# Optimization experiments

Measured on AMD Instinct MI355X. Metric: run time of the kernel, lower is better.

## Reference

```python
import jax, jax.numpy as jnp
import numpy as np

SCALING = 32.0 / 16.0  # alpha / rank

def setup_inputs() -> dict:
    key = jax.random.key(0)
    ks = jax.random.split(key, 6)
    B, S, D_IN, D_OUT, R, N_ADAPT = 32, 1024, 1024, 4096, 16, 8
    hidden_states = jax.random.normal(ks[0], (B, S, D_IN), dtype=jnp.float32)
    adapter_ids = jax.random.randint(ks[1], (B,), 0, N_ADAPT, dtype=jnp.int32)
    W = jax.random.normal(ks[2], (D_IN, D_OUT), dtype=jnp.float32) * 0.02
    bias = jax.random.normal(ks[3], (D_OUT,), dtype=jnp.float32) * 0.02
    lora_a = jax.random.normal(ks[4], (N_ADAPT, D_IN, R), dtype=jnp.float32) * (1.0 / np.sqrt(D_IN))
    lora_b = jax.random.normal(ks[5], (N_ADAPT, R, D_OUT), dtype=jnp.float32) * 0.02
    return {"hidden_states": hidden_states, "adapter_ids": adapter_ids,
            "W": W, "bias": bias, "lora_a": lora_a, "lora_b": lora_b}

def reference(hidden_states, adapter_ids, W, bias, lora_a, lora_b):
    # Base GPT-2 Conv1D: x @ W + b, W: [in, out]
    base_out = jnp.einsum('bsd,do->bso', hidden_states, W) + bias
    # Per-sample routed LoRA: gather each sample's adapter A/B, then batched low-rank matmuls.
    # Equivalent to the torch loop over unique adapter ids with mask/scatter (dropout=0, eval).
    a_sel = lora_a[adapter_ids]  # [B, d_in, r]
    b_sel = lora_b[adapter_ids]  # [B, r, d_out]
    low_rank = jnp.einsum('bsd,bdr->bsr', hidden_states, a_sel)
    delta = jnp.einsum('bsr,bro->bso', low_rank, b_sel) * SCALING
    return base_out + delta
```

## Files before the change

### kernel.cpp

```cpp
#include <hip/hip_runtime.h>
#include <hip/hip_bf16.h>
#include <stdint.h>

constexpr int kB = 32;
constexpr int kS = 1024;
constexpr int kDin = 1024;
constexpr int kDout = 4096;
constexpr int kRank = 16;
constexpr int kNAdapt = 8;
constexpr int kM = kB * kS;
constexpr float kScale = 2.0f;

typedef __attribute__((ext_vector_type(4))) float f32x4;
typedef __attribute__((ext_vector_type(8))) short s16x8;
typedef __attribute__((ext_vector_type(8))) unsigned short u16x8;
typedef __attribute__((ext_vector_type(4))) unsigned short u16x4;

__device__ __forceinline__ unsigned short f2bf(float f) {
  union { float f; uint32_t u; } x; x.f = f;
  uint32_t u = x.u;
  u += 0x7fffu + ((u >> 16) & 1u);
  return (unsigned short)(u >> 16);
}

__global__ void cast_h_kernel(const float* __restrict__ h, unsigned short* __restrict__ out) {
  size_t i = (size_t)blockIdx.x * blockDim.x + threadIdx.x;
  const f32x4* src = reinterpret_cast<const f32x4*>(h) + i * 2;
  f32x4 v0 = src[0], v1 = src[1];
  u16x8 r;
  r[0] = f2bf(v0[0]); r[1] = f2bf(v0[1]); r[2] = f2bf(v0[2]); r[3] = f2bf(v0[3]);
  r[4] = f2bf(v1[0]); r[5] = f2bf(v1[1]); r[6] = f2bf(v1[2]); r[7] = f2bf(v1[3]);
  *reinterpret_cast<u16x8*>(out + i * 8) = r;
}

__global__ __launch_bounds__(256) void build_weff_kernel(
    const float* __restrict__ W,
    const float* __restrict__ la,
    const float* __restrict__ lb,
    unsigned short* __restrict__ weff) {
  __shared__ float Wt[64][68];
  __shared__ float At[64][20];
  __shared__ float Bt[16][68];
  int bid = blockIdx.x;
  int e = bid & 7;
  int rem = bid >> 3;
  int dt = rem >> 6;
  int ot = rem & 63;
  int d0 = dt * 64, o0 = ot * 64;
  int t = threadIdx.x;
  {
    int r = t >> 4;
    int c = (t & 15) * 4;
    const float* wp = W + (size_t)(d0 + r) * kDout + o0 + c;
#pragma unroll
    for (int p = 0; p < 4; ++p) {
      f32x4 v = *reinterpret_cast<const f32x4*>(wp + (size_t)p * 16 * kDout);
      *reinterpret_cast<f32x4*>(&Wt[p * 16 + r][c]) = v;
    }
  }
  {
    int d = t >> 2, r4 = (t & 3) * 4;
    f32x4 v = *reinterpret_cast<const f32x4*>(la + ((size_t)e * kDin + d0 + d) * kRank + r4);
    *reinterpret_cast<f32x4*>(&At[d][r4]) = v;
  }
  {
    int r = t >> 4, c = (t & 15) * 4;
    f32x4 v = *reinterpret_cast<const f32x4*>(lb + ((size_t)e * kRank + r) * kDout + o0 + c);
    *reinterpret_cast<f32x4*>(&Bt[r][c]) = v;
  }
  __syncthreads();
  int ol_base = t >> 4;
  int dl = (t & 15) * 4;
  f32x4 areg[4][4];
#pragma unroll
  for (int j = 0; j < 4; ++j)
#pragma unroll
    for (int q = 0; q < 4; ++q)
      areg[j][q] = *reinterpret_cast<const f32x4*>(&At[dl + j][q * 4]);
#pragma unroll
  for (int p = 0; p < 4; ++p) {
    int ol = p * 16 + ol_base;
    float bv[kRank];
#pragma unroll
    for (int r = 0; r < kRank; ++r) bv[r] = Bt[r][ol];
    u16x4 r4;
#pragma unroll
    for (int j = 0; j < 4; ++j) {
      float acc = 0.f;
#pragma unroll
      for (int q = 0; q < 4; ++q)
        acc += areg[j][q][0] * bv[q * 4 + 0] + areg[j][q][1] * bv[q * 4 + 1] +
               areg[j][q][2] * bv[q * 4 + 2] + areg[j][q][3] * bv[q * 4 + 3];
      r4[j] = f2bf(Wt[dl + j][ol] + kScale * acc);
    }
    *reinterpret_cast<u16x4*>(weff + ((size_t)e * kDout + o0 + ol) * kDin + d0 + dl) = r4;
  }
}

constexpr int BM = 256, BN = 256, BK = 64;
constexpr int MT2 = kM / BM;
constexpr int NT2 = kDout / BN;
constexpr int NWG2 = MT2 * NT2;
constexpr int KT = kDin / BK;

__device__ __forceinline__ void gload16(const unsigned short* g, unsigned short* l) {
  __builtin_amdgcn_global_load_lds((const __attribute__((address_space(1))) void*)g,
                                   (__attribute__((address_space(3))) void*)l, 16, 0, 0);
}

#define STG_A(slot, h, kt) do { \
  gload16(gA + (size_t)((h) * 128) * kDin + (kt) * 64, ldst + (slot) * 32768 + (h) * 8192); \
  gload16(gA + (size_t)((h) * 128 + 64) * kDin + (kt) * 64, ldst + (slot) * 32768 + (h) * 8192 + 4096); \
} while (0)
#define STG_B(slot, h, kt) do { \
  gload16(gB + (size_t)((h) * 128) * kDin + (kt) * 64, ldst + (slot) * 32768 + 16384 + (h) * 8192); \
  gload16(gB + (size_t)((h) * 128 + 64) * kDin + (kt) * 64, ldst + (slot) * 32768 + 16384 + (h) * 8192 + 4096); \
} while (0)

#define RD_A(mh) do { _Pragma("unroll") for (int i = 0; i < 4; ++i) { \
  a[i][0] = *(const s16x8*)&lds[sBase + aRow + ((mh) * 4 + i) * 1024 + e0]; \
  a[i][1] = *(const s16x8*)&lds[sBase + aRow + ((mh) * 4 + i) * 1024 + e1]; } } while (0)
#define RD_B(nh, breg) do { _Pragma("unroll") for (int j = 0; j < 2; ++j) { \
  breg[j][0] = *(const s16x8*)&lds[sBase + bRow + ((nh) * 2 + j) * 1024 + e0]; \
  breg[j][1] = *(const s16x8*)&lds[sBase + bRow + ((nh) * 2 + j) * 1024 + e1]; } } while (0)

#define MM(mh, nh, breg) do { \
  __builtin_amdgcn_s_setprio(1); \
  _Pragma("unroll") for (int i = 0; i < 4; ++i) \
  _Pragma("unroll") for (int j = 0; j < 2; ++j) { \
    acc[(mh) * 4 + i][(nh) * 2 + j] = __builtin_amdgcn_mfma_f32_16x16x32_bf16( \
        a[i][0], breg[j][0], acc[(mh) * 4 + i][(nh) * 2 + j], 0, 0, 0); \
    acc[(mh) * 4 + i][(nh) * 2 + j] = __builtin_amdgcn_mfma_f32_16x16x32_bf16( \
        a[i][1], breg[j][1], acc[(mh) * 4 + i][(nh) * 2 + j], 0, 0, 0); } \
  __builtin_amdgcn_s_setprio(0); \
} while (0)

#define BAR1() do { __builtin_amdgcn_sched_barrier(0); __builtin_amdgcn_s_barrier(); \
  asm volatile("s_waitcnt lgkmcnt(0)" ::: "memory"); __builtin_amdgcn_sched_barrier(0); } while (0)
#define BAR2() do { __builtin_amdgcn_sched_barrier(0); __builtin_amdgcn_s_barrier(); } while (0)
#define VMC(n) asm volatile("s_waitcnt vmcnt(" #n ")" ::: "memory")

#define ITER(iv, LAST_) do { \
  int kt1 = 2 * (iv) + 1, kt2 = 2 * (iv) + 2, kt3 = 2 * (iv) + 3; \
  (void)kt2; (void)kt3; \
  { int sBase = 0; RD_A(0); RD_B(0, b0); } \
  STG_B(1, 1, kt1); \
  BAR1(); MM(0, 0, b0); BAR2(); \
  { int sBase = 0; RD_B(1, b1); } \
  STG_A(1, 1, kt1); \
  BAR1(); MM(0, 1, b1); BAR2(); \
  { int sBase = 0; RD_A(1); } \
  if (!LAST_) STG_B(0, 0, kt2); \
  BAR1(); MM(1, 0, b0); BAR2(); \
  if (!LAST_) { STG_A(0, 0, kt2); VMC(4); } else { VMC(0); } \
  BAR1(); MM(1, 1, b1); BAR2(); \
  { int sBase = 32768; RD_A(0); RD_B(0, b0); } \
  if (!LAST_) STG_B(0, 1, kt2); \
  BAR1(); MM(0, 0, b0); BAR2(); \
  { int sBase = 32768; RD_B(1, b1); } \
  if (!LAST_) STG_A(0, 1, kt2); \
  BAR1(); MM(0, 1, b1); BAR2(); \
  { int sBase = 32768; RD_A(1); } \
  if (!LAST_) STG_B(1, 0, kt3); \
  BAR1(); MM(1, 0, b0); BAR2(); \
  if (!LAST_) { STG_A(1, 0, kt3); VMC(4); } \
  BAR1(); MM(1, 1, b1); BAR2(); \
} while (0)

__global__ __launch_bounds__(512, 2) void gemm256_kernel(
    const unsigned short* __restrict__ Ab,
    const unsigned short* __restrict__ Weff,
    const float* __restrict__ bias,
    const int* __restrict__ aids,
    float* __restrict__ out) {
  __shared__ unsigned short lds[65536];
  int bid = blockIdx.x;
  int swz = (bid & 7) * (NWG2 / 8) + (bid >> 3);
  int mt = swz >> 4, nt = swz & 15;
  int aid = aids[mt >> 2];
  const unsigned short* Aptr = Ab + (size_t)mt * BM * kDin;
  const unsigned short* Bptr = Weff + ((size_t)aid * kDout + (size_t)nt * BN) * kDin;

  int t = threadIdx.x;
  int l = t & 63;
  int w = t >> 6;
  int wm = w >> 2;
  int wn = w & 3;

  int srcColEl = ((t & 7) * 8) ^ (((t >> 3) & 7) << 3);
  const unsigned short* gA = Aptr + (size_t)(t >> 3) * kDin + srcColEl;
  const unsigned short* gB = Bptr + (size_t)(t >> 3) * kDin + srcColEl;
  unsigned short* ldst = lds + t * 8;

  int xmEl = (l & 7) << 3;
  int e0 = (((l >> 4) * 8) ^ xmEl);
  int e1 = e0 ^ 32;
  int aRow = (wm * 128 + (l & 15)) * 64;
  int bRow = (wn * 64 + (l & 15)) * 64 + 16384;

  f32x4 acc[8][4];
#pragma unroll
  for (int m = 0; m < 8; ++m)
#pragma unroll
    for (int n = 0; n < 4; ++n) acc[m][n] = f32x4{0.f, 0.f, 0.f, 0.f};
  s16x8 a[4][2], b0[2][2], b1[2][2];

  STG_B(0, 0, 0); STG_A(0, 0, 0); STG_B(0, 1, 0); STG_A(0, 1, 0);
  STG_B(1, 0, 1); STG_A(1, 0, 1);
  VMC(4);
  BAR2();

  for (int i = 0; i < 7; ++i) ITER(i, false);
  ITER(7, true);

  size_t row0 = (size_t)mt * BM + wm * 128 + (l >> 4) * 4;
  int col0 = nt * BN + wn * 64 + (l & 15);
#pragma unroll
  for (int nf = 0; nf < 4; ++nf) {
    float bv = bias[col0 + nf * 16];
#pragma unroll
    for (int mf = 0; mf < 8; ++mf) {
#pragma unroll
      for (int j = 0; j < 4; ++j)
        out[(row0 + mf * 16 + j) * kDout + col0 + nf * 16] = acc[mf][nf][j] + bv;
    }
  }
}

extern "C" void kernel_launch(void* const* d_in, const int* in_sizes, int n_in,
                              void* d_out, int out_size, void* d_ws, size_t ws_size,
                              hipStream_t stream) {
  const float* h    = (const float*)d_in[0];
  const int*   aids = (const int*)d_in[1];
  const float* W    = (const float*)d_in[2];
  const float* bias = (const float*)d_in[3];
  const float* la   = (const float*)d_in[4];
  const float* lb   = (const float*)d_in[5];
  float* out = (float*)d_out;

  unsigned short* Abf  = (unsigned short*)d_ws;
  unsigned short* Weff = Abf + (size_t)kM * kDin;

  cast_h_kernel<<<(kM * (size_t)kDin / 8) / 256, 256, 0, stream>>>(h, Abf);
  build_weff_kernel<<<kNAdapt * (kDin / 64) * (kDout / 64), 256, 0, stream>>>(W, la, lb, Weff);
  gemm256_kernel<<<NWG2, 512, 0, stream>>>(Abf, Weff, bias, aids, out);
}
```

Measured before the change: 460.7 us.

## Make GEMM persistent over eight N-tiles per block with cross-tile prefetch

Each workgroup now computes eight consecutive 256-wide output tiles for one M tile, which cuts the grid from 2048 to 256 blocks. The K-loop prefetch continues into the next tile's B panel and the first A k-slices, so the pipeline does not drain between tiles. The aim is to remove prologue/epilogue bubbles and launch/tail overhead, and to keep the A panel hot in cache. In exchange, the output stores are serialized inside each block, and with only 256 blocks of 512 threads some CUs may be underfilled, with poorer load balance.

```diff
diff --git a/kernel.cpp b/kernel.cpp
--- a/kernel.cpp
+++ b/kernel.cpp
@@ -100,38 +100,38 @@
 constexpr int BM = 256, BN = 256, BK = 64;
 constexpr int MT2 = kM / BM;
 constexpr int NT2 = kDout / BN;
-constexpr int NWG2 = MT2 * NT2;
-constexpr int KT = kDin / BK;
+constexpr int TPB = 8;
+constexpr int NBLK = MT2 * NT2 / TPB;
 
 __device__ __forceinline__ void gload16(const unsigned short* g, unsigned short* l) {
   __builtin_amdgcn_global_load_lds((const __attribute__((address_space(1))) void*)g,
                                    (__attribute__((address_space(3))) void*)l, 16, 0, 0);
 }
 
-#define STG_A(slot, h, kt) do { \
-  gload16(gA + (size_t)((h) * 128) * kDin + (kt) * 64, ldst + (slot) * 32768 + (h) * 8192); \
-  gload16(gA + (size_t)((h) * 128 + 64) * kDin + (kt) * 64, ldst + (slot) * 32768 + (h) * 8192 + 4096); \
+#define STG_A2(slot, h, kk) do { \
+  gload16(gA + (size_t)((h) * 128) * kDin + ((kk) & 15) * 64, ldst + (slot) * 32768 + (h) * 8192); \
+  gload16(gA + (size_t)((h) * 128 + 64) * kDin + ((kk) & 15) * 64, ldst + (slot) * 32768 + (h) * 8192 + 4096); \
 } while (0)
-#define STG_B(slot, h, kt) do { \
-  gload16(gB + (size_t)((h) * 128) * kDin + (kt) * 64, ldst + (slot) * 32768 + 16384 + (h) * 8192); \
-  gload16(gB + (size_t)((h) * 128 + 64) * kDin + (kt) * 64, ldst + (slot) * 32768 + 16384 + (h) * 8192 + 4096); \
+#define STG_B2(slot, h, kk, BP) do { \
+  gload16((BP) + (size_t)((h) * 128) * kDin + ((kk) & 15) * 64, ldst + (slot) * 32768 + 16384 + (h) * 8192); \
+  gload16((BP) + (size_t)((h) * 128 + 64) * kDin + ((kk) & 15) * 64, ldst + (slot) * 32768 + 16384 + (h) * 8192 + 4096); \
 } while (0)
 
-#define RD_A(mh) do { _Pragma("unroll") for (int i = 0; i < 4; ++i) { \
-  a[i][0] = *(const s16x8*)&lds[sBase + aRow + ((mh) * 4 + i) * 1024 + e0]; \
-  a[i][1] = *(const s16x8*)&lds[sBase + aRow + ((mh) * 4 + i) * 1024 + e1]; } } while (0)
-#define RD_B(nh, breg) do { _Pragma("unroll") for (int j = 0; j < 2; ++j) { \
-  breg[j][0] = *(const s16x8*)&lds[sBase + bRow + ((nh) * 2 + j) * 1024 + e0]; \
-  breg[j][1] = *(const s16x8*)&lds[sBase + bRow + ((nh) * 2 + j) * 1024 + e1]; } } while (0)
+#define RD_A(mh) do { _Pragma("unroll") for (int ii = 0; ii < 4; ++ii) { \
+  a[ii][0] = *(const s16x8*)&lds[sBase + aRow + ((mh) * 4 + ii) * 1024 + e0]; \
+  a[ii][1] = *(const s16x8*)&lds[sBase + aRow + ((mh) * 4 + ii) * 1024 + e1]; } } while (0)
+#define RD_B(nh, breg) do { _Pragma("unroll") for (int jj = 0; jj < 2; ++jj) { \
+  breg[jj][0] = *(const s16x8*)&lds[sBase + bRow + ((nh) * 2 + jj) * 1024 + e0]; \
+  breg[jj][1] = *(const s16x8*)&lds[sBase + bRow + ((nh) * 2 + jj) * 1024 + e1]; } } while (0)
 
 #define MM(mh, nh, breg) do { \
   __builtin_amdgcn_s_setprio(1); \
-  _Pragma("unroll") for (int i = 0; i < 4; ++i) \
-  _Pragma("unroll") for (int j = 0; j < 2; ++j) { \
-    acc[(mh) * 4 + i][(nh) * 2 + j] = __builtin_amdgcn_mfma_f32_16x16x32_bf16( \
-        a[i][0], breg[j][0], acc[(mh) * 4 + i][(nh) * 2 + j], 0, 0, 0); \
-    acc[(mh) * 4 + i][(nh) * 2 + j] = __builtin_amdgcn_mfma_f32_16x16x32_bf16( \
-        a[i][1], breg[j][1], acc[(mh) * 4 + i][(nh) * 2 + j], 0, 0, 0); } \
+  _Pragma("unroll") for (int ii = 0; ii < 4; ++ii) \
+  _Pragma("unroll") for (int jj = 0; jj < 2; ++jj) { \
+    acc[(mh) * 4 + ii][(nh) * 2 + jj] = __builtin_amdgcn_mfma_f32_16x16x32_bf16( \
+        a[ii][0], breg[jj][0], acc[(mh) * 4 + ii][(nh) * 2 + jj], 0, 0, 0); \
+    acc[(mh) * 4 + ii][(nh) * 2 + jj] = __builtin_amdgcn_mfma_f32_16x16x32_bf16( \
+        a[ii][1], breg[jj][1], acc[(mh) * 4 + ii][(nh) * 2 + jj], 0, 0, 0); } \
   __builtin_amdgcn_s_setprio(0); \
 } while (0)
 
@@ -139,33 +139,6 @@
   asm volatile("s_waitcnt lgkmcnt(0)" ::: "memory"); __builtin_amdgcn_sched_barrier(0); } while (0)
 #define BAR2() do { __builtin_amdgcn_sched_barrier(0); __builtin_amdgcn_s_barrier(); } while (0)
 #define VMC(n) asm volatile("s_waitcnt vmcnt(" #n ")" ::: "memory")
-
-#define ITER(iv, LAST_) do { \
-  int kt1 = 2 * (iv) + 1, kt2 = 2 * (iv) + 2, kt3 = 2 * (iv) + 3; \
-  (void)kt2; (void)kt3; \
-  { int sBase = 0; RD_A(0); RD_B(0, b0); } \
-  STG_B(1, 1, kt1); \
-  BAR1(); MM(0, 0, b0); BAR2(); \
-  { int sBase = 0; RD_B(1, b1); } \
-  STG_A(1, 1, kt1); \
-  BAR1(); MM(0, 1, b1); BAR2(); \
-  { int sBase = 0; RD_A(1); } \
-  if (!LAST_) STG_B(0, 0, kt2); \
-  BAR1(); MM(1, 0, b0); BAR2(); \
-  if (!LAST_) { STG_A(0, 0, kt2); VMC(4); } else { VMC(0); } \
-  BAR1(); MM(1, 1, b1); BAR2(); \
-  { int sBase = 32768; RD_A(0); RD_B(0, b0); } \
-  if (!LAST_) STG_B(0, 1, kt2); \
-  BAR1(); MM(0, 0, b0); BAR2(); \
-  { int sBase = 32768; RD_B(1, b1); } \
-  if (!LAST_) STG_A(0, 1, kt2); \
-  BAR1(); MM(0, 1, b1); BAR2(); \
-  { int sBase = 32768; RD_A(1); } \
-  if (!LAST_) STG_B(1, 0, kt3); \
-  BAR1(); MM(1, 0, b0); BAR2(); \
-  if (!LAST_) { STG_A(1, 0, kt3); VMC(4); } \
-  BAR1(); MM(1, 1, b1); BAR2(); \
-} while (0)
 
 __global__ __launch_bounds__(512, 2) void gemm256_kernel(
     const unsigned short* __restrict__ Ab,
@@ -174,12 +147,11 @@
     const int* __restrict__ aids,
     float* __restrict__ out) {
   __shared__ unsigned short lds[65536];
-  int bid = blockIdx.x;
-  int swz = (bid & 7) * (NWG2 / 8) + (bid >> 3);
-  int mt = swz >> 4, nt = swz & 15;
+  int b = blockIdx.x;
+  int mt = (b & 7) * 16 + (b >> 4);
+  int o8 = (b >> 3) & 1;
   int aid = aids[mt >> 2];
   const unsigned short* Aptr = Ab + (size_t)mt * BM * kDin;
-  const unsigned short* Bptr = Weff + ((size_t)aid * kDout + (size_t)nt * BN) * kDin;
 
   int t = threadIdx.x;
   int l = t & 63;
@@ -189,7 +161,10 @@
 
   int srcColEl = ((t & 7) * 8) ^ (((t >> 3) & 7) << 3);
   const unsigned short* gA = Aptr + (size_t)(t >> 3) * kDin + srcColEl;
-  const unsigned short* gB = Bptr + (size_t)(t >> 3) * kDin + srcColEl;
+  const unsigned short* bP =
+      Weff + ((size_t)aid * kDout + (size_t)(o8 * 8) * BN) * kDin +
+      (size_t)(t >> 3) * kDin + srcColEl;
+  constexpr size_t panelStride = (size_t)BN * kDin;
   unsigned short* ldst = lds + t * 8;
 
   int xmEl = (l & 7) << 3;
@@ -205,25 +180,68 @@
     for (int n = 0; n < 4; ++n) acc[m][n] = f32x4{0.f, 0.f, 0.f, 0.f};
   s16x8 a[4][2], b0[2][2], b1[2][2];
 
-  STG_B(0, 0, 0); STG_A(0, 0, 0); STG_B(0, 1, 0); STG_A(0, 1, 0);
-  STG_B(1, 0, 1); STG_A(1, 0, 1);
+  size_t row0 = (size_t)mt * BM + wm * 128 + (l >> 4) * 4;
+  int colBase = (o8 * 8) * BN + wn * 64 + (l & 15);
+  size_t outOff = row0 * kDout + colBase;
+
+  STG_B2(0, 0, 0, bP); STG_A2(0, 0, 0); STG_B2(0, 1, 0, bP); STG_A2(0, 1, 0);
+  STG_B2(1, 0, 1, bP); STG_A2(1, 0, 1);
   VMC(4);
   BAR2();
 
-  for (int i = 0; i < 7; ++i) ITER(i, false);
-  ITER(7, true);
-
-  size_t row0 = (size_t)mt * BM + wm * 128 + (l >> 4) * 4;
-  int col0 = nt * BN + wn * 64 + (l & 15);
-#pragma unroll
-  for (int nf = 0; nf < 4; ++nf) {
-    float bv = bias[col0 + nf * 16];
-#pragma unroll
-    for (int mf = 0; mf < 8; ++mf) {
-#pragma unroll
-      for (int j = 0; j < 4; ++j)
-        out[(row0 + mf * 16 + j) * kDout + col0 + nf * 16] = acc[mf][nf][j] + bv;
-    }
+#pragma unroll 1
+  for (int tt = 0; tt < TPB; ++tt) {
+    const unsigned short* bN = bP + panelStride;
+    const bool lastTile = (tt == TPB - 1);
+#pragma unroll
+    for (int i = 0; i < 8; ++i) {
+      const int kt1 = 2 * i + 1, kt2 = 2 * i + 2, kt3 = 2 * i + 3;
+      const bool cross = (i == 7);
+      { int sBase = 0; RD_A(0); RD_B(0, b0); }
+      STG_B2(1, 1, kt1, bP);
+      BAR1(); MM(0, 0, b0); BAR2();
+      { int sBase = 0; RD_B(1, b1); }
+      STG_A2(1, 1, kt1);
+      BAR1(); MM(0, 1, b1); BAR2();
+      { int sBase = 0; RD_A(1); }
+      if (!cross) STG_B2(0, 0, kt2, bP);
+      else if (!lastTile) STG_B2(0, 0, kt2, bN);
+      BAR1(); MM(1, 0, b0); BAR2();
+      if (!cross || !lastTile) { STG_A2(0, 0, kt2); VMC(4); }
+      else { VMC(0); }
+      BAR1(); MM(1, 1, b1); BAR2();
+      { int sBase = 32768; RD_A(0); RD_B(0, b0); }
+      if (!cross) STG_B2(0, 1, kt2, bP);
+      else if (!lastTile) STG_B2(0, 1, kt2, bN);
+      BAR1(); MM(0, 0, b0); BAR2();
+      { int sBase = 32768; RD_B(1, b1); }
+      if (!cross || !lastTile) STG_A2(0, 1, kt2);
+      BAR1(); MM(0, 1, b1); BAR2();
+      { int sBase = 32768; RD_A(1); }
+      if (!cross) STG_B2(1, 0, kt3, bP);
+      else if (!lastTile) STG_B2(1, 0, kt3, bN);
+      BAR1(); MM(1, 0, b0); BAR2();
+      if (!cross || !lastTile) { STG_A2(1, 0, kt3); VMC(4); }
+      BAR1(); MM(1, 1, b1); BAR2();
+    }
+#pragma unroll
+    for (int nf = 0; nf < 4; ++nf) {
+      float bv = bias[colBase + tt * BN + nf * 16];
+#pragma unroll
+      for (int mf = 0; mf < 8; ++mf) {
+#pragma unroll
+        for (int j = 0; j < 4; ++j)
+          out[outOff + (size_t)tt * BN + (size_t)(mf * 16 + j) * kDout + nf * 16] =
+              acc[mf][nf][j] + bv;
+      }
+    }
+    if (!lastTile) {
+#pragma unroll
+      for (int m = 0; m < 8; ++m)
+#pragma unroll
+        for (int n = 0; n < 4; ++n) acc[m][n] = f32x4{0.f, 0.f, 0.f, 0.f};
+    }
+    bP = bN;
   }
 }
 
@@ -243,5 +261,5 @@
 
   cast_h_kernel<<<(kM * (size_t)kDin / 8) / 256, 256, 0, stream>>>(h, Abf);
   build_weff_kernel<<<kNAdapt * (kDin / 64) * (kDout / 64), 256, 0, stream>>>(W, la, lb, Weff);
-  gemm256_kernel<<<NWG2, 512, 0, stream>>>(Abf, Weff, bias, aids, out);
-}
+  gemm256_kernel<<<NBLK, 512, 0, stream>>>(Abf, Weff, bias, aids, out);
+}
```

Result: slower. 767.1 us (+66.5%).

## Triple-buffer B tiles in LDS while keeping A double-buffered

Applied to the files above, without the earlier changes.

Splits LDS into two A slots and three B slots (160KB total), so B tiles are prefetched two k-steps ahead. The main loop is now fully unrolled and uses modular slot indices for B. The goal is to hide global-load latency for the weight operand behind more MFMA work. The cost is more LDS per block, which may not fit two 512-thread blocks per CU and could lower occupancy.

```diff
diff --git a/kernel.cpp b/kernel.cpp
--- a/kernel.cpp
+++ b/kernel.cpp
@@ -101,37 +101,36 @@
 constexpr int MT2 = kM / BM;
 constexpr int NT2 = kDout / BN;
 constexpr int NWG2 = MT2 * NT2;
-constexpr int KT = kDin / BK;
 
 __device__ __forceinline__ void gload16(const unsigned short* g, unsigned short* l) {
   __builtin_amdgcn_global_load_lds((const __attribute__((address_space(1))) void*)g,
                                    (__attribute__((address_space(3))) void*)l, 16, 0, 0);
 }
 
-#define STG_A(slot, h, kt) do { \
-  gload16(gA + (size_t)((h) * 128) * kDin + (kt) * 64, ldst + (slot) * 32768 + (h) * 8192); \
-  gload16(gA + (size_t)((h) * 128 + 64) * kDin + (kt) * 64, ldst + (slot) * 32768 + (h) * 8192 + 4096); \
+#define STG_A3(sa, h, kk) do { \
+  gload16(gA + (size_t)((h) * 128) * kDin + (kk) * 64, ldst + (sa) * 16384 + (h) * 8192); \
+  gload16(gA + (size_t)((h) * 128 + 64) * kDin + (kk) * 64, ldst + (sa) * 16384 + (h) * 8192 + 4096); \
 } while (0)
-#define STG_B(slot, h, kt) do { \
-  gload16(gB + (size_t)((h) * 128) * kDin + (kt) * 64, ldst + (slot) * 32768 + 16384 + (h) * 8192); \
-  gload16(gB + (size_t)((h) * 128 + 64) * kDin + (kt) * 64, ldst + (slot) * 32768 + 16384 + (h) * 8192 + 4096); \
+#define STG_B3(sb, h, kk) do { \
+  gload16(gB + (size_t)((h) * 128) * kDin + (kk) * 64, ldst + 32768 + (sb) * 16384 + (h) * 8192); \
+  gload16(gB + (size_t)((h) * 128 + 64) * kDin + (kk) * 64, ldst + 32768 + (sb) * 16384 + (h) * 8192 + 4096); \
 } while (0)
 
-#define RD_A(mh) do { _Pragma("unroll") for (int i = 0; i < 4; ++i) { \
-  a[i][0] = *(const s16x8*)&lds[sBase + aRow + ((mh) * 4 + i) * 1024 + e0]; \
-  a[i][1] = *(const s16x8*)&lds[sBase + aRow + ((mh) * 4 + i) * 1024 + e1]; } } while (0)
-#define RD_B(nh, breg) do { _Pragma("unroll") for (int j = 0; j < 2; ++j) { \
-  breg[j][0] = *(const s16x8*)&lds[sBase + bRow + ((nh) * 2 + j) * 1024 + e0]; \
-  breg[j][1] = *(const s16x8*)&lds[sBase + bRow + ((nh) * 2 + j) * 1024 + e1]; } } while (0)
+#define RD_A(mh, sa) do { _Pragma("unroll") for (int ii = 0; ii < 4; ++ii) { \
+  a[ii][0] = *(const s16x8*)&lds[(sa) * 16384 + aRow + ((mh) * 4 + ii) * 1024 + e0]; \
+  a[ii][1] = *(const s16x8*)&lds[(sa) * 16384 + aRow + ((mh) * 4 + ii) * 1024 + e1]; } } while (0)
+#define RD_B(nh, breg, sb) do { _Pragma("unroll") for (int jj = 0; jj < 2; ++jj) { \
+  breg[jj][0] = *(const s16x8*)&lds[32768 + (sb) * 16384 + bRow + ((nh) * 2 + jj) * 1024 + e0]; \
+  breg[jj][1] = *(const s16x8*)&lds[32768 + (sb) * 16384 + bRow + ((nh) * 2 + jj) * 1024 + e1]; } } while (0)
 
 #define MM(mh, nh, breg) do { \
   __builtin_amdgcn_s_setprio(1); \
-  _Pragma("unroll") for (int i = 0; i < 4; ++i) \
-  _Pragma("unroll") for (int j = 0; j < 2; ++j) { \
-    acc[(mh) * 4 + i][(nh) * 2 + j] = __builtin_amdgcn_mfma_f32_16x16x32_bf16( \
-        a[i][0], breg[j][0], acc[(mh) * 4 + i][(nh) * 2 + j], 0, 0, 0); \
-    acc[(mh) * 4 + i][(nh) * 2 + j] = __builtin_amdgcn_mfma_f32_16x16x32_bf16( \
-        a[i][1], breg[j][1], acc[(mh) * 4 + i][(nh) * 2 + j], 0, 0, 0); } \
+  _Pragma("unroll") for (int ii = 0; ii < 4; ++ii) \
+  _Pragma("unroll") for (int jj = 0; jj < 2; ++jj) { \
+    acc[(mh) * 4 + ii][(nh) * 2 + jj] = __builtin_amdgcn_mfma_f32_16x16x32_bf16( \
+        a[ii][0], breg[jj][0], acc[(mh) * 4 + ii][(nh) * 2 + jj], 0, 0, 0); \
+    acc[(mh) * 4 + ii][(nh) * 2 + jj] = __builtin_amdgcn_mfma_f32_16x16x32_bf16( \
+        a[ii][1], breg[jj][1], acc[(mh) * 4 + ii][(nh) * 2 + jj], 0, 0, 0); } \
   __builtin_amdgcn_s_setprio(0); \
 } while (0)
 
@@ -139,33 +138,6 @@
   asm volatile("s_waitcnt lgkmcnt(0)" ::: "memory"); __builtin_amdgcn_sched_barrier(0); } while (0)
 #define BAR2() do { __builtin_amdgcn_sched_barrier(0); __builtin_amdgcn_s_barrier(); } while (0)
 #define VMC(n) asm volatile("s_waitcnt vmcnt(" #n ")" ::: "memory")
-
-#define ITER(iv, LAST_) do { \
-  int kt1 = 2 * (iv) + 1, kt2 = 2 * (iv) + 2, kt3 = 2 * (iv) + 3; \
-  (void)kt2; (void)kt3; \
-  { int sBase = 0; RD_A(0); RD_B(0, b0); } \
-  STG_B(1, 1, kt1); \
-  BAR1(); MM(0, 0, b0); BAR2(); \
-  { int sBase = 0; RD_B(1, b1); } \
-  STG_A(1, 1, kt1); \
-  BAR1(); MM(0, 1, b1); BAR2(); \
-  { int sBase = 0; RD_A(1); } \
-  if (!LAST_) STG_B(0, 0, kt2); \
-  BAR1(); MM(1, 0, b0); BAR2(); \
-  if (!LAST_) { STG_A(0, 0, kt2); VMC(4); } else { VMC(0); } \
-  BAR1(); MM(1, 1, b1); BAR2(); \
-  { int sBase = 32768; RD_A(0); RD_B(0, b0); } \
-  if (!LAST_) STG_B(0, 1, kt2); \
-  BAR1(); MM(0, 0, b0); BAR2(); \
-  { int sBase = 32768; RD_B(1, b1); } \
-  if (!LAST_) STG_A(0, 1, kt2); \
-  BAR1(); MM(0, 1, b1); BAR2(); \
-  { int sBase = 32768; RD_A(1); } \
-  if (!LAST_) STG_B(1, 0, kt3); \
-  BAR1(); MM(1, 0, b0); BAR2(); \
-  if (!LAST_) { STG_A(1, 0, kt3); VMC(4); } \
-  BAR1(); MM(1, 1, b1); BAR2(); \
-} while (0)
 
 __global__ __launch_bounds__(512, 2) void gemm256_kernel(
     const unsigned short* __restrict__ Ab,
@@ -173,7 +145,7 @@
     const float* __restrict__ bias,
     const int* __restrict__ aids,
     float* __restrict__ out) {
-  __shared__ unsigned short lds[65536];
+  __shared__ unsigned short lds[81920];
   int bid = blockIdx.x;
   int swz = (bid & 7) * (NWG2 / 8) + (bid >> 3);
   int mt = swz >> 4, nt = swz & 15;
@@ -196,7 +168,7 @@
   int e0 = (((l >> 4) * 8) ^ xmEl);
   int e1 = e0 ^ 32;
   int aRow = (wm * 128 + (l & 15)) * 64;
-  int bRow = (wn * 64 + (l & 15)) * 64 + 16384;
+  int bRow = (wn * 64 + (l & 15)) * 64;
 
   f32x4 acc[8][4];
 #pragma unroll
@@ -205,13 +177,40 @@
     for (int n = 0; n < 4; ++n) acc[m][n] = f32x4{0.f, 0.f, 0.f, 0.f};
   s16x8 a[4][2], b0[2][2], b1[2][2];
 
-  STG_B(0, 0, 0); STG_A(0, 0, 0); STG_B(0, 1, 0); STG_A(0, 1, 0);
-  STG_B(1, 0, 1); STG_A(1, 0, 1);
-  VMC(4);
+  STG_B3(0, 0, 0); STG_B3(0, 1, 0); STG_A3(0, 0, 0); STG_A3(0, 1, 0);
+  STG_B3(1, 0, 1); STG_B3(1, 1, 1); STG_A3(1, 0, 1);
+  VMC(6);
   BAR2();
 
-  for (int i = 0; i < 7; ++i) ITER(i, false);
-  ITER(7, true);
+#pragma unroll
+  for (int i = 0; i < 8; ++i) {
+    const int kt0 = 2 * i, kt1 = 2 * i + 1;
+    const int sb0 = kt0 % 3, sb1 = kt1 % 3;
+    const int sb2 = (kt0 + 2) % 3, sb3 = (kt1 + 2) % 3;
+    const bool last = (i == 7);
+    RD_A(0, 0); RD_B(0, b0, sb0);
+    if (!last) STG_B3(sb2, 0, kt0 + 2);
+    BAR1(); MM(0, 0, b0); BAR2();
+    RD_B(1, b1, sb0);
+    STG_A3(1, 1, kt1);
+    BAR1(); MM(0, 1, b1); BAR2();
+    RD_A(1, 0);
+    if (!last) STG_B3(sb2, 1, kt0 + 2);
+    BAR1(); MM(1, 0, b0); BAR2();
+    if (!last) { STG_A3(0, 0, kt0 + 2); VMC(4); } else { VMC(0); }
+    BAR1(); MM(1, 1, b1); BAR2();
+    RD_A(0, 1); RD_B(0, b0, sb1);
+    if (!last) STG_B3(sb3, 0, kt1 + 2);
+    BAR1(); MM(0, 0, b0); BAR2();
+    RD_B(1, b1, sb1);
+    if (!last) STG_A3(0, 1, kt0 + 2);
+    BAR1(); MM(0, 1, b1); BAR2();
+    RD_A(1, 1);
+    if (!last) STG_B3(sb3, 1, kt1 + 2);
+    BAR1(); MM(1, 0, b0); BAR2();
+    if (!last) { STG_A3(1, 0, kt1 + 2); VMC(4); }
+    BAR1(); MM(1, 1, b1); BAR2();
+  }
 
   size_t row0 = (size_t)mt * BM + wm * 128 + (l >> 4) * 4;
   int col0 = nt * BN + wn * 64 + (l & 15);
```

After: 459.5 us. No clear change (-0.2%).
